# Kernel optimization log

Hardware: AMD Instinct MI355X
Metric: run time of the kernel (lower is better)

## Reference

```python
import jax, jax.numpy as jnp
import numpy as np

GROUP = 16
RANK = 32
ALPHA = 32.0
SCALING = ALPHA / RANK  # alpha = lora_dim -> 1.0
DIM = 1024
NLAYERS = 18
EPS = 1e-5


def setup_inputs() -> dict:
    key = jax.random.key(0)
    ks = jax.random.split(key, 6)
    x = jax.random.normal(ks[0], (16384, DIM), dtype=jnp.float32)
    qweight = jax.random.randint(ks[1], (NLAYERS, DIM, DIM), 0, 16, dtype=jnp.int32)
    scales = jax.random.uniform(ks[2], (NLAYERS, DIM, DIM // GROUP), dtype=jnp.float32)
    bias = jax.random.normal(ks[3], (NLAYERS, DIM), dtype=jnp.float32)
    lora_a = jax.random.normal(ks[4], (NLAYERS, RANK, DIM), dtype=jnp.float32)
    lora_b = jax.random.normal(ks[5], (NLAYERS, DIM, RANK), dtype=jnp.float32)
    ln_gamma = jnp.ones((5, DIM), dtype=jnp.float32)
    ln_beta = jnp.zeros((5, DIM), dtype=jnp.float32)
    return {"x": x, "qweight": qweight, "scales": scales, "bias": bias,
            "lora_a": lora_a, "lora_b": lora_b, "ln_gamma": ln_gamma, "ln_beta": ln_beta}


def _dequant(q, s):
    # q: [O, I] int4 values stored 0..15; s: [O, I//GROUP] group scales
    O, I = q.shape
    w = (q.astype(jnp.float32) - 8.0).reshape(O, I // GROUP, GROUP) * s[:, :, None]
    return w.reshape(O, I)


def _qlora_linear(h, q, s, b, la, lb):
    w = _dequant(q, s)                              # [O, I]
    base = h @ w.T + b                              # dequant-matmul
    lora = (h @ la.T) @ lb.T                        # rank-32 adapter
    return base + SCALING * lora


def _layernorm(h, g, b):
    mu = jnp.mean(h, axis=-1, keepdims=True)
    var = jnp.mean(jnp.square(h - mu), axis=-1, keepdims=True)
    return (h - mu) * jax.lax.rsqrt(var + EPS) * g + b


def reference(x, qweight, scales, bias, lora_a, lora_b, ln_gamma, ln_beta):
    h = x
    li = 0
    for blk in range(6):
        r = h
        for j in range(3):
            r = _qlora_linear(r, qweight[li], scales[li], bias[li], lora_a[li], lora_b[li])
            li += 1
            if j < 2:
                r = jax.nn.relu(r)
        h = h + r  # residual per Block
        if blk < 5:
            h = _layernorm(h, ln_gamma[blk], ln_beta[blk])
    return h
```

## Files before the change

kernel.cpp:

```cpp
#include <hip/hip_runtime.h>

#define DIM 1024
#define MROWS 16384
#define NLAYERS 18
#define RANK 32
#define GROUPSZ 16

typedef _Float16 f16_t;
typedef __attribute__((ext_vector_type(8))) _Float16 f16x8;
typedef __attribute__((ext_vector_type(4))) _Float16 f16x4;
typedef __attribute__((ext_vector_type(4))) float f32x4;

__device__ __forceinline__ float h2f(f16_t h) { return (float)h; }
__device__ __forceinline__ f16_t f2h(float f) { return (f16_t)f; }

__global__ __launch_bounds__(256) void prep_weights(
    const int* __restrict__ qw, const float* __restrict__ scales,
    const float* __restrict__ la, const float* __restrict__ lb,
    f16_t* __restrict__ weff)
{
    const int blk = blockIdx.x;
    const int layer = blk >> 7;
    const int o0 = (blk & 127) * 8;
    const int t = threadIdx.x;
    __shared__ float lbs[8][32];
    lbs[t >> 5][t & 31] = lb[((size_t)layer * DIM + o0) * RANK + t];
    const int i0 = t * 4;
    const size_t wbase = (size_t)layer * DIM * DIM;

    int4 q4[8];
    float sc[8];
#pragma unroll
    for (int o = 0; o < 8; ++o) {
        q4[o] = *(const int4*)(qw + wbase + (size_t)(o0 + o) * DIM + i0);
        sc[o] = scales[((size_t)layer * DIM + o0 + o) * (DIM / GROUPSZ) + (i0 >> 4)];
    }
    __syncthreads();

    float acc[8][4];
#pragma unroll
    for (int o = 0; o < 8; ++o)
#pragma unroll
        for (int k = 0; k < 4; ++k) acc[o][k] = 0.f;
    const float* lap = la + (size_t)layer * RANK * DIM + i0;
#pragma unroll 8
    for (int r = 0; r < RANK; ++r) {
        float4 a4 = *(const float4*)(lap + (size_t)r * DIM);
#pragma unroll
        for (int o = 0; o < 8; ++o) {
            float f = lbs[o][r];
            acc[o][0] += f * a4.x; acc[o][1] += f * a4.y;
            acc[o][2] += f * a4.z; acc[o][3] += f * a4.w;
        }
    }
#pragma unroll
    for (int o = 0; o < 8; ++o) {
        f16x4 w;
        w[0] = f2h((float)(q4[o].x - 8) * sc[o] + acc[o][0]);
        w[1] = f2h((float)(q4[o].y - 8) * sc[o] + acc[o][1]);
        w[2] = f2h((float)(q4[o].z - 8) * sc[o] + acc[o][2]);
        w[3] = f2h((float)(q4[o].w - 8) * sc[o] + acc[o][3]);
        *(f16x4*)(weff + wbase + (size_t)(o0 + o) * DIM + i0) = w;
    }
}

__global__ __launch_bounds__(256) void cvt_f32_f16(const float* __restrict__ in,
                                                   f16_t* __restrict__ out, int n)
{
    const int i = (blockIdx.x * 256 + threadIdx.x) * 4;
    if (i < n) {
        float4 v = *(const float4*)(in + i);
        f16x4 o;
        o[0] = f2h(v.x); o[1] = f2h(v.y); o[2] = f2h(v.z); o[3] = f2h(v.w);
        *(f16x4*)(out + i) = o;
    }
}

template <int EPI>
__global__ __launch_bounds__(512, 1) void gemm_bt(
    const f16_t* __restrict__ A, const f16_t* __restrict__ W,
    const float* __restrict__ bias, const f16_t* __restrict__ res,
    f16_t* __restrict__ outb, float* __restrict__ outf,
    float sA, float sB)
{
    constexpr int BM = 256, BN = 256, BK = 64, K = DIM;
    constexpr int KT = K / BK;
    __shared__ __align__(16) f16_t As[2][BM * BK];
    __shared__ __align__(16) f16_t Bs[2][BN * BK];

    const int tid = threadIdx.x;
    const int bid = blockIdx.x;
    const int nid = ((bid & 7) << 5) + (bid >> 3);
    const int m0 = (nid >> 2) * BM;
    const int n0 = (nid & 3) * BN;

    const int wave = tid >> 6, lane = tid & 63;
    const int wm = wave >> 2;
    const int wn = wave & 3;
    const int lr = lane & 15;
    const int l4 = lane >> 4;

    f32x4 acc[8][4];
#pragma unroll
    for (int i = 0; i < 8; ++i)
#pragma unroll
        for (int j = 0; j < 4; ++j) acc[i][j] = (f32x4){0.f, 0.f, 0.f, 0.f};

    const int rs = tid >> 3;
    const int cs = ((tid & 7) ^ (rs & 7)) * 8;
    const f16_t* Ag = A + (size_t)(m0 + rs) * K + cs;
    const f16_t* Wg = W + (size_t)(n0 + rs) * K + cs;

#define STAGE(kt_, buf_)                                                          \
    {                                                                             \
        const int kb_ = (kt_) * BK;                                               \
        f16_t* ad_ = &As[buf_][0] + tid * 8;                                      \
        f16_t* bd_ = &Bs[buf_][0] + tid * 8;                                      \
        _Pragma("unroll")                                                         \
        for (int j_ = 0; j_ < 4; ++j_)                                            \
            __builtin_amdgcn_global_load_lds(                                     \
                (const __attribute__((address_space(1))) void*)(Ag + (size_t)(j_ * 64) * K + kb_), \
                (__attribute__((address_space(3))) void*)(ad_ + j_ * 4096), 16, 0, 0); \
        _Pragma("unroll")                                                         \
        for (int j_ = 0; j_ < 4; ++j_)                                            \
            __builtin_amdgcn_global_load_lds(                                     \
                (const __attribute__((address_space(1))) void*)(Wg + (size_t)(j_ * 64) * K + kb_), \
                (__attribute__((address_space(3))) void*)(bd_ + j_ * 4096), 16, 0, 0); \
    }

    STAGE(0, 0);
    STAGE(1, 1);

    for (int kt = 0; kt < KT; ++kt) {
        if (kt < KT - 1) asm volatile("s_waitcnt vmcnt(8)" ::: "memory");
        else             asm volatile("s_waitcnt vmcnt(0)" ::: "memory");
        __builtin_amdgcn_s_barrier();

        const f16_t* ab = &As[kt & 1][0];
        const f16_t* bb = &Bs[kt & 1][0];
#pragma unroll
        for (int kk = 0; kk < 2; ++kk) {
            f16x8 bfr[4];
#pragma unroll
            for (int fn = 0; fn < 4; ++fn) {
                const int row = wn * 64 + fn * 16 + lr;
                const int chunk = ((kk * 4 + l4) ^ (row & 7)) * 8;
                bfr[fn] = *(const f16x8*)&bb[row * BK + chunk];
            }
            f16x8 af[8];
#pragma unroll
            for (int fm = 0; fm < 8; ++fm) {
                const int row = wm * 128 + fm * 16 + lr;
                const int chunk = ((kk * 4 + l4) ^ (row & 7)) * 8;
                af[fm] = *(const f16x8*)&ab[row * BK + chunk];
            }
#pragma unroll
            for (int fm = 0; fm < 8; ++fm)
#pragma unroll
                for (int fn = 0; fn < 4; ++fn)
                    acc[fm][fn] = __builtin_amdgcn_mfma_f32_16x16x32_f16(
                        af[fm], bfr[fn], acc[fm][fn], 0, 0, 0);
        }
        __builtin_amdgcn_s_barrier();
        if (kt + 2 < KT) STAGE(kt + 2, kt & 1);
    }
#undef STAGE

    const int crow0 = m0 + wm * 128 + l4 * 4;
    const int ccol0 = n0 + wn * 64;
#pragma unroll
    for (int fm = 0; fm < 8; ++fm) {
#pragma unroll
        for (int fn = 0; fn < 4; ++fn) {
            const int col = ccol0 + fn * 16 + lr;
            const float bcol = bias[col];
#pragma unroll
            for (int j = 0; j < 4; ++j) {
                const int row = crow0 + fm * 16 + j;
                float v;
                if (EPI == 0) {
                    v = acc[fm][fn][j] * sA + bcol * sB;
                    v = fmaxf(v, 0.f);
                    outb[(size_t)row * DIM + col] = f2h(v);
                } else {
                    const float rv = h2f(res[(size_t)row * DIM + col]);
                    v = acc[fm][fn][j] * sA + (bcol + rv) * sB;
                    if (EPI == 1) outb[(size_t)row * DIM + col] = f2h(v);
                    else          outf[(size_t)row * DIM + col] = v;
                }
            }
        }
    }
}

__global__ __launch_bounds__(256) void ln_kernel(const f16_t* __restrict__ in,
                                                 f16_t* __restrict__ out,
                                                 const float* __restrict__ gamma,
                                                 const float* __restrict__ beta)
{
    const int row = blockIdx.x;
    const int t = threadIdx.x;
    const int c = t * 4;
    f16x4 v4 = *(const f16x4*)(in + (size_t)row * DIM + c);
    float h0 = h2f(v4[0]), h1 = h2f(v4[1]), h2 = h2f(v4[2]), h3 = h2f(v4[3]);
    float s = h0 + h1 + h2 + h3;
    float sq = h0 * h0 + h1 * h1 + h2 * h2 + h3 * h3;
#pragma unroll
    for (int off = 32; off > 0; off >>= 1) {
        s += __shfl_down(s, off);
        sq += __shfl_down(sq, off);
    }
    __shared__ float ss[4], ssq[4];
    const int wave = t >> 6, lane = t & 63;
    if (lane == 0) { ss[wave] = s; ssq[wave] = sq; }
    __syncthreads();
    s = ss[0] + ss[1] + ss[2] + ss[3];
    sq = ssq[0] + ssq[1] + ssq[2] + ssq[3];
    const float mu = s * (1.f / DIM);
    const float var = sq * (1.f / DIM) - mu * mu;
    const float rs = rsqrtf(var + 1e-5f);
    float4 g = *(const float4*)(gamma + c);
    float4 b = *(const float4*)(beta + c);
    f16x4 o;
    o[0] = f2h((h0 - mu) * rs * g.x + b.x);
    o[1] = f2h((h1 - mu) * rs * g.y + b.y);
    o[2] = f2h((h2 - mu) * rs * g.z + b.z);
    o[3] = f2h((h3 - mu) * rs * g.w + b.w);
    *(f16x4*)(out + (size_t)row * DIM + c) = o;
}

extern "C" void kernel_launch(void* const* d_in, const int* in_sizes, int n_in,
                              void* d_out, int out_size, void* d_ws, size_t ws_size,
                              hipStream_t stream)
{
    const float* x      = (const float*)d_in[0];
    const int* qw       = (const int*)d_in[1];
    const float* scales = (const float*)d_in[2];
    const float* bias   = (const float*)d_in[3];
    const float* la     = (const float*)d_in[4];
    const float* lb     = (const float*)d_in[5];
    const float* g      = (const float*)d_in[6];
    const float* be     = (const float*)d_in[7];
    float* out = (float*)d_out;

    char* ws = (char*)d_ws;
    const size_t WEFF_BYTES = (size_t)NLAYERS * DIM * DIM * 2;
    const size_t ACT_BYTES  = (size_t)MROWS * DIM * 2;
    f16_t* weff = (f16_t*)ws;
    f16_t* hbuf = (f16_t*)(ws + WEFF_BYTES);
    f16_t* t1   = (f16_t*)(ws + WEFF_BYTES + ACT_BYTES);
    f16_t* t2   = (f16_t*)(ws + WEFF_BYTES + 2 * ACT_BYTES);

    prep_weights<<<dim3(NLAYERS * 128), 256, 0, stream>>>(qw, scales, la, lb, weff);
    cvt_f32_f16<<<dim3((MROWS * DIM) / 1024), 256, 0, stream>>>(x, hbuf, MROWS * DIM);

    const dim3 ggrid(256);
    for (int blk = 0; blk < 6; ++blk) {
        const int li = blk * 3;
        const size_t w0 = (size_t)li * DIM * DIM;
        gemm_bt<0><<<ggrid, 512, 0, stream>>>(hbuf, weff + w0, bias + (size_t)li * DIM,
                                              nullptr, t1, nullptr, 1.f / 16.f, 1.f / 16.f);
        gemm_bt<0><<<ggrid, 512, 0, stream>>>(t1, weff + w0 + (size_t)DIM * DIM,
                                              bias + (size_t)(li + 1) * DIM, nullptr, t2, nullptr,
                                              1.f / 64.f, 1.f / 1024.f);
        if (blk < 5) {
            gemm_bt<1><<<ggrid, 512, 0, stream>>>(t2, weff + w0 + 2 * (size_t)DIM * DIM,
                                                  bias + (size_t)(li + 2) * DIM, hbuf, t1, nullptr,
                                                  1.f, 1.f / 1024.f);
            ln_kernel<<<dim3(MROWS), 256, 0, stream>>>(t1, hbuf, g + (size_t)blk * DIM,
                                                       be + (size_t)blk * DIM);
        } else {
            gemm_bt<2><<<ggrid, 512, 0, stream>>>(t2, weff + w0 + 2 * (size_t)DIM * DIM,
                                                  bias + (size_t)(li + 2) * DIM, hbuf, nullptr, out,
                                                  1024.f, 1.f);
        }
    }
}
```

Measured before the change: 955.0 us.

## Deepen GEMM K-pipeline to four LDS stages with split A/B staging

```diff
diff --git a/kernel.cpp b/kernel.cpp
--- a/kernel.cpp
+++ b/kernel.cpp
@@ -83,22 +83,23 @@
     f16_t* __restrict__ outb, float* __restrict__ outf,
     float sA, float sB)
 {
-    constexpr int BM = 256, BN = 256, BK = 64, K = DIM;
+    constexpr int BK = 32, K = DIM;
     constexpr int KT = K / BK;
-    __shared__ __align__(16) f16_t As[2][BM * BK];
-    __shared__ __align__(16) f16_t Bs[2][BN * BK];
+    __shared__ __align__(16) f16_t As[4][256 * BK];
+    __shared__ __align__(16) f16_t Bs[4][256 * BK];
 
     const int tid = threadIdx.x;
     const int bid = blockIdx.x;
     const int nid = ((bid & 7) << 5) + (bid >> 3);
-    const int m0 = (nid >> 2) * BM;
-    const int n0 = (nid & 3) * BN;
+    const int m0 = (nid >> 2) * 256;
+    const int n0 = (nid & 3) * 256;
 
     const int wave = tid >> 6, lane = tid & 63;
     const int wm = wave >> 2;
     const int wn = wave & 3;
     const int lr = lane & 15;
     const int l4 = lane >> 4;
+    const int cfrag = ((l4 ^ (lr & 3)) * 8);
 
     f32x4 acc[8][4];
 #pragma unroll
@@ -106,65 +107,89 @@
 #pragma unroll
         for (int j = 0; j < 4; ++j) acc[i][j] = (f32x4){0.f, 0.f, 0.f, 0.f};
 
-    const int rs = tid >> 3;
-    const int cs = ((tid & 7) ^ (rs & 7)) * 8;
+    const int rs = tid >> 2;
+    const int cs = ((tid & 3) ^ (rs & 3)) * 8;
     const f16_t* Ag = A + (size_t)(m0 + rs) * K + cs;
     const f16_t* Wg = W + (size_t)(n0 + rs) * K + cs;
 
-#define STAGE(kt_, buf_)                                                          \
-    {                                                                             \
-        const int kb_ = (kt_) * BK;                                               \
-        f16_t* ad_ = &As[buf_][0] + tid * 8;                                      \
-        f16_t* bd_ = &Bs[buf_][0] + tid * 8;                                      \
-        _Pragma("unroll")                                                         \
-        for (int j_ = 0; j_ < 4; ++j_)                                            \
-            __builtin_amdgcn_global_load_lds(                                     \
-                (const __attribute__((address_space(1))) void*)(Ag + (size_t)(j_ * 64) * K + kb_), \
-                (__attribute__((address_space(3))) void*)(ad_ + j_ * 4096), 16, 0, 0); \
-        _Pragma("unroll")                                                         \
-        for (int j_ = 0; j_ < 4; ++j_)                                            \
-            __builtin_amdgcn_global_load_lds(                                     \
-                (const __attribute__((address_space(1))) void*)(Wg + (size_t)(j_ * 64) * K + kb_), \
-                (__attribute__((address_space(3))) void*)(bd_ + j_ * 4096), 16, 0, 0); \
-    }
-
-    STAGE(0, 0);
-    STAGE(1, 1);
-
-    for (int kt = 0; kt < KT; ++kt) {
-        if (kt < KT - 1) asm volatile("s_waitcnt vmcnt(8)" ::: "memory");
-        else             asm volatile("s_waitcnt vmcnt(0)" ::: "memory");
-        __builtin_amdgcn_s_barrier();
-
-        const f16_t* ab = &As[kt & 1][0];
-        const f16_t* bb = &Bs[kt & 1][0];
-#pragma unroll
-        for (int kk = 0; kk < 2; ++kk) {
-            f16x8 bfr[4];
-#pragma unroll
-            for (int fn = 0; fn < 4; ++fn) {
-                const int row = wn * 64 + fn * 16 + lr;
-                const int chunk = ((kk * 4 + l4) ^ (row & 7)) * 8;
-                bfr[fn] = *(const f16x8*)&bb[row * BK + chunk];
-            }
-            f16x8 af[8];
-#pragma unroll
-            for (int fm = 0; fm < 8; ++fm) {
-                const int row = wm * 128 + fm * 16 + lr;
-                const int chunk = ((kk * 4 + l4) ^ (row & 7)) * 8;
-                af[fm] = *(const f16x8*)&ab[row * BK + chunk];
-            }
-#pragma unroll
-            for (int fm = 0; fm < 8; ++fm)
+#define GLL(src_, dst_)                                                     \
+    __builtin_amdgcn_global_load_lds(                                       \
+        (const __attribute__((address_space(1))) void*)(src_),              \
+        (__attribute__((address_space(3))) void*)(dst_), 16, 0, 0)
+#define STAGE_A(kt_, b_)                                                    \
+    {                                                                       \
+        const int kb_ = (kt_) * BK;                                         \
+        f16_t* d_ = &As[b_][0] + tid * 8;                                   \
+        GLL(Ag + kb_, d_);                                                  \
+        GLL(Ag + (size_t)128 * K + kb_, d_ + 4096);                         \
+    }
+#define STAGE_B(kt_, b_)                                                    \
+    {                                                                       \
+        const int kb_ = (kt_) * BK;                                         \
+        f16_t* d_ = &Bs[b_][0] + tid * 8;                                   \
+        GLL(Wg + kb_, d_);                                                  \
+        GLL(Wg + (size_t)128 * K + kb_, d_ + 4096);                         \
+    }
+
+    STAGE_A(0, 0); STAGE_B(0, 0);
+    STAGE_A(1, 1); STAGE_B(1, 1);
+    STAGE_A(2, 2); STAGE_B(2, 2);
+    asm volatile("s_waitcnt vmcnt(8)" ::: "memory");
+    __builtin_amdgcn_s_barrier();
+
+    const int arow = wm * 128 + lr;
+    const int brow = wn * 64 + lr;
+
+    for (int j = 0; j < KT; ++j) {
+        const f16_t* ab = &As[j & 3][0];
+        const f16_t* bb = &Bs[j & 3][0];
+        const bool st = (j + 3 < KT);
+        const int b3 = (j + 3) & 3;
+
+        if (st) STAGE_A(j + 3, b3);
+        f16x8 bfr[4];
+#pragma unroll
+        for (int fn = 0; fn < 4; ++fn)
+            bfr[fn] = *(const f16x8*)&bb[(brow + fn * 16) * BK + cfrag];
+        {
+            f16x8 af[4];
+#pragma unroll
+            for (int fm = 0; fm < 4; ++fm)
+                af[fm] = *(const f16x8*)&ab[(arow + fm * 16) * BK + cfrag];
+            __builtin_amdgcn_s_setprio(1);
+#pragma unroll
+            for (int fm = 0; fm < 4; ++fm)
 #pragma unroll
                 for (int fn = 0; fn < 4; ++fn)
                     acc[fm][fn] = __builtin_amdgcn_mfma_f32_16x16x32_f16(
                         af[fm], bfr[fn], acc[fm][fn], 0, 0, 0);
+            __builtin_amdgcn_s_setprio(0);
         }
         __builtin_amdgcn_s_barrier();
-        if (kt + 2 < KT) STAGE(kt + 2, kt & 1);
-    }
-#undef STAGE
+
+        if (st) STAGE_B(j + 3, b3);
+        {
+            f16x8 af[4];
+#pragma unroll
+            for (int fm = 0; fm < 4; ++fm)
+                af[fm] = *(const f16x8*)&ab[(arow + 64 + fm * 16) * BK + cfrag];
+            __builtin_amdgcn_s_setprio(1);
+#pragma unroll
+            for (int fm = 0; fm < 4; ++fm)
+#pragma unroll
+                for (int fn = 0; fn < 4; ++fn)
+                    acc[fm + 4][fn] = __builtin_amdgcn_mfma_f32_16x16x32_f16(
+                        af[fm], bfr[fn], acc[fm + 4][fn], 0, 0, 0);
+            __builtin_amdgcn_s_setprio(0);
+        }
+        if (j < KT - 3)       asm volatile("s_waitcnt vmcnt(8)" ::: "memory");
+        else if (j == KT - 3) asm volatile("s_waitcnt vmcnt(4)" ::: "memory");
+        else if (j == KT - 2) asm volatile("s_waitcnt vmcnt(0)" ::: "memory");
+        __builtin_amdgcn_s_barrier();
+    }
+#undef STAGE_A
+#undef STAGE_B
+#undef GLL
 
     const int crow0 = m0 + wm * 128 + l4 * 4;
     const int ccol0 = n0 + wn * 64;
```

Result: no change. 973.1 us (+1.9%).
